# Kernel optimization log

Measured on AMD Instinct MI355X. Metric: run time of the kernel, lower is better.

The kernel has to match this reference:

```python
import jax, jax.numpy as jnp
import numpy as np

H = 8           # hidden_size
IN = 1          # input_size
OUT = 1         # output_size
T_IN = 512      # input_length
T_OUT = 128     # output_length
B = 65536       # batch


def _gru_cell(x, h, W_ih, W_hh, b_ih, b_hh):
    # torch.nn.GRUCell math. x: [B, D], h: [B, H]
    gi = x @ W_ih.T + b_ih          # [B, 3H]
    gh = h @ W_hh.T + b_hh          # [B, 3H]
    i_r, i_z, i_n = jnp.split(gi, 3, axis=-1)
    h_r, h_z, h_n = jnp.split(gh, 3, axis=-1)
    r = jax.nn.sigmoid(i_r + h_r)
    z = jax.nn.sigmoid(i_z + h_z)
    n = jnp.tanh(i_n + r * h_n)
    return (1.0 - z) * n + z * h


def setup_inputs() -> dict:
    key = jax.random.key(0)
    ks = jax.random.split(key, 12)
    s_in = 1.0 / np.sqrt(H)
    x = jax.random.normal(ks[0], (T_IN, B, IN), dtype=jnp.float32)
    u = lambda k, shp: jax.random.uniform(k, shp, dtype=jnp.float32, minval=-s_in, maxval=s_in)
    return {
        "x": x,
        "enc_W_ih": u(ks[1], (3 * H, IN)),
        "enc_W_hh": u(ks[2], (3 * H, H)),
        "enc_b_ih": u(ks[3], (3 * H,)),
        "enc_b_hh": u(ks[4], (3 * H,)),
        "dec_W_ih": u(ks[5], (3 * H, OUT)),
        "dec_W_hh": u(ks[6], (3 * H, H)),
        "dec_b_ih": u(ks[7], (3 * H,)),
        "dec_b_hh": u(ks[8], (3 * H,)),
        "fc_W": u(ks[9], (OUT, H)),
        "fc_b": u(ks[10], (OUT,)),
    }


def reference(x, enc_W_ih, enc_W_hh, enc_b_ih, enc_b_hh,
              dec_W_ih, dec_W_hh, dec_b_ih, dec_b_hh, fc_W, fc_b):
    batch = x.shape[1]
    h0 = jnp.zeros((batch, H), dtype=x.dtype)

    def enc_step(h, x_t):
        return _gru_cell(x_t, h, enc_W_ih, enc_W_hh, enc_b_ih, enc_b_hh), None

    enc_h, _ = jax.lax.scan(enc_step, h0, x)

    def dec_step(carry, _):
        h, inp = carry
        h = _gru_cell(inp, h, dec_W_ih, dec_W_hh, dec_b_ih, dec_b_hh)
        out_t = h @ fc_W.T + fc_b      # [B, OUT]
        return (h, out_t), out_t

    # decoder_feat is None, teacher_forcing False: feed back own prediction
    _, outs = jax.lax.scan(dec_step, (enc_h, x[-1]), None, length=T_OUT)
    return outs  # [T_OUT, B, OUT]
```

## Files before the change

### kernel.cpp

```cpp
#include <hip/hip_runtime.h>

#define T_IN   512
#define T_OUT  128
#define BATCH  65536

typedef float v2f __attribute__((ext_vector_type(2)));

__device__ __forceinline__ float exp2_fast(float v) { return __builtin_amdgcn_exp2f(v); }
__device__ __forceinline__ float rcp_fast(float v)  { return __builtin_amdgcn_rcpf(v); }

__device__ __forceinline__ v2f pk_fma(v2f a, v2f b, v2f c) {
    v2f d;
    asm("v_pk_fma_f32 %0, %1, %2, %3" : "=v"(d) : "v"(a), "v"(b), "v"(c));
    return d;
}

template<int CTRL>
__device__ __forceinline__ float dppf(float v) {
    return __int_as_float(__builtin_amdgcn_mov_dpp(__float_as_int(v), CTRL, 0xF, 0xF, false));
}
#define QP_XOR1 0xB1
#define QP_XOR2 0x4E
#define QP_XOR3 0x1B
#define HALF_MIRROR 0x141

__global__ __launch_bounds__(256, 4) void gru_seq2seq(
    const float* __restrict__ x,
    const float* __restrict__ eWih, const float* __restrict__ eWhh,
    const float* __restrict__ eBih, const float* __restrict__ eBhh,
    const float* __restrict__ dWih, const float* __restrict__ dWhh,
    const float* __restrict__ dBih, const float* __restrict__ dBhh,
    const float* __restrict__ fcW,  const float* __restrict__ fcB,
    float* __restrict__ out)
{
    const int tid = threadIdx.x;
    const int u   = tid & 7;
    const int e0  = (int)blockIdx.x * 64 + (tid >> 3);

    const float CR = -1.44269504088896340736f;
    const float CN =  2.88539008177792681472f;

    v2f wr[8], wz[8], wn[8];
    v2f wirv, wizv, winv;
    v2f brv, bzv, bnv, binv;

    auto dup = [](float v) { return v2f{v, v}; };

    auto load_w = [&](const float* Wih, const float* Whh,
                      const float* Bih, const float* Bhh) {
        #pragma unroll
        for (int d = 0; d < 8; ++d) {
            const int c = u ^ d;
            wr[d] = dup(Whh[u*8      + c] * CR);
            wz[d] = dup(Whh[(u+8)*8  + c] * CR);
            wn[d] = dup(Whh[(u+16)*8 + c] * CN);
        }
        wirv = dup(Wih[u]    * CR);
        wizv = dup(Wih[u+8]  * CR);
        winv = dup(Wih[u+16] * CN);
        brv  = dup((Bih[u]   + Bhh[u])   * CR);
        bzv  = dup((Bih[u+8] + Bhh[u+8]) * CR);
        bnv  = dup(Bhh[u+16] * CN);
        binv = dup(Bih[u+16] * CN);
    };

    load_w(eWih, eWhh, eBih, eBhh);

    const v2f C_NEG2 = {-2.f, -2.f};
    const v2f C_ONE  = { 1.f,  1.f};

    v2f hp[8];
    #pragma unroll
    for (int d = 0; d < 8; ++d) hp[d] = v2f{0.f, 0.f};

    auto cell2 = [&](v2f xp) {
        v2f ar = brv, az = bzv, an = bnv;
        #pragma unroll
        for (int d = 0; d < 8; ++d) {
            ar = pk_fma(wr[d], hp[d], ar);
            az = pk_fma(wz[d], hp[d], az);
            an = pk_fma(wn[d], hp[d], an);
        }
        const v2f sr = pk_fma(xp, wirv, ar);
        const v2f sz = pk_fma(xp, wizv, az);

        const float er0 = exp2_fast(sr.x), er1 = exp2_fast(sr.y);
        const float ez0 = exp2_fast(sz.x), ez1 = exp2_fast(sz.y);
        const float dr0 = 1.0f + er0, dr1 = 1.0f + er1;
        const float dz0 = 1.0f + ez0, dz1 = 1.0f + ez1;
        const float P0  = dr0 * dz0,  P1  = dr1 * dz1;
        const float rp  = rcp_fast(P0 * P1);
        const float rpA = rp * P1,    rpB = rp * P0;
        const v2f r01 = { dz0 * rpA, dz1 * rpB };
        const v2f z01 = { dr0 * rpA, dr1 * rpB };

        v2f pre = pk_fma(xp, winv, binv);
        pre = pk_fma(r01, an, pre);
        const float en0 = exp2_fast(pre.x), en1 = exp2_fast(pre.y);
        const float Dn0 = 1.0f + en0, Dn1 = 1.0f + en1;
        const float rpn = rcp_fast(Dn0 * Dn1);
        const v2f rn  = { rpn * Dn1, rpn * Dn0 };
        const v2f n01 = pk_fma(C_NEG2, rn, C_ONE);

        const v2f hm = hp[0] - n01;
        hp[0] = pk_fma(z01, hm, n01);

        const float g0 = hp[0].x, g1 = hp[0].y;
        float a7x = dppf<HALF_MIRROR>(g0);
        float a7y = dppf<HALF_MIRROR>(g1);
        hp[1] = v2f{ dppf<QP_XOR1>(g0), dppf<QP_XOR1>(g1) };
        hp[2] = v2f{ dppf<QP_XOR2>(g0), dppf<QP_XOR2>(g1) };
        hp[3] = v2f{ dppf<QP_XOR3>(g0), dppf<QP_XOR3>(g1) };
        hp[7] = v2f{ a7x, a7y };
        hp[6] = v2f{ dppf<QP_XOR1>(a7x), dppf<QP_XOR1>(a7y) };
        hp[5] = v2f{ dppf<QP_XOR2>(a7x), dppf<QP_XOR2>(a7y) };
        hp[4] = v2f{ dppf<QP_XOR3>(a7x), dppf<QP_XOR3>(a7y) };
    };

    const float* xp = x + e0;
    v2f xa0 = { xp[0],     xp[32] };
    v2f xa1 = { xp[BATCH], xp[BATCH + 32] };
    xp += 2 * (size_t)BATCH;
    #pragma unroll 2
    for (int t = 0; t < T_IN - 2; ++t) {
        const v2f xa2 = { xp[0], xp[32] };
        xp += BATCH;
        cell2(xa0);
        xa0 = xa1; xa1 = xa2;
    }
    cell2(xa0);
    cell2(xa1);

    load_w(dWih, dWhh, dBih, dBhh);
    v2f fw[8];
    #pragma unroll
    for (int d = 0; d < 8; ++d) fw[d] = dup(fcW[u ^ d]);
    const v2f fbv = dup(fcB[0]);

    v2f inp = xa1;
    float* outp = out + e0;
    #pragma unroll 1
    for (int t = 0; t < T_OUT; ++t) {
        cell2(inp);
        v2f ay = fbv;
        #pragma unroll
        for (int d = 0; d < 8; ++d) ay = pk_fma(fw[d], hp[d], ay);
        if (u == 0) {
            outp[t * BATCH]      = ay.x;
            outp[t * BATCH + 32] = ay.y;
        }
        inp = ay;
    }
}

extern "C" void kernel_launch(void* const* d_in, const int* in_sizes, int n_in,
                              void* d_out, int out_size, void* d_ws, size_t ws_size,
                              hipStream_t stream) {
    const float* x    = (const float*)d_in[0];
    const float* eWih = (const float*)d_in[1];
    const float* eWhh = (const float*)d_in[2];
    const float* eBih = (const float*)d_in[3];
    const float* eBhh = (const float*)d_in[4];
    const float* dWih = (const float*)d_in[5];
    const float* dWhh = (const float*)d_in[6];
    const float* dBih = (const float*)d_in[7];
    const float* dBhh = (const float*)d_in[8];
    const float* fcW  = (const float*)d_in[9];
    const float* fcB  = (const float*)d_in[10];
    float* out = (float*)d_out;

    dim3 grid(BATCH / 64);
    dim3 block(256);
    gru_seq2seq<<<grid, block, 0, stream>>>(x, eWih, eWhh, eBih, eBhh,
                                            dWih, dWhh, dBih, dBhh,
                                            fcW, fcB, out);
}
```

Before: 382.5 us.

## Remap GRU lanes to two hidden units per lane over four-lane groups

Each batch element is now handled by a group of 4 lanes, with every lane owning 2 hidden units packed into a v2f. Before, 8 lanes each owned 1 unit for 2 batch elements. The recurrent matvec uses op_sel variants of v_pk_fma to broadcast one half of each neighbour's hidden pair. This cuts the per-step hidden-state exchange from 14 DPP moves to 6. The decoder's output projection becomes one packed multiply plus a two-step DPP reduction instead of 16 packed FMAs. The cost is a more intricate weight layout, and transcendental work per lane is unchanged.

```diff
diff --git a/kernel.cpp b/kernel.cpp
--- a/kernel.cpp
+++ b/kernel.cpp
@@ -6,12 +6,39 @@
 
 typedef float v2f __attribute__((ext_vector_type(2)));
 
+__device__ __forceinline__ float rcp_fast(float v) { return __builtin_amdgcn_rcpf(v); }
 __device__ __forceinline__ float exp2_fast(float v) { return __builtin_amdgcn_exp2f(v); }
-__device__ __forceinline__ float rcp_fast(float v)  { return __builtin_amdgcn_rcpf(v); }
 
 __device__ __forceinline__ v2f pk_fma(v2f a, v2f b, v2f c) {
     v2f d;
     asm("v_pk_fma_f32 %0, %1, %2, %3" : "=v"(d) : "v"(a), "v"(b), "v"(c));
+    return d;
+}
+__device__ __forceinline__ void pk_fma_ip(v2f& acc, v2f a, v2f b) {
+    asm("v_pk_fma_f32 %0, %1, %2, %0" : "+v"(acc) : "v"(a), "v"(b));
+}
+__device__ __forceinline__ v2f pk_mul(v2f a, v2f b) {
+    v2f d;
+    asm("v_pk_mul_f32 %0, %1, %2" : "=v"(d) : "v"(a), "v"(b));
+    return d;
+}
+__device__ __forceinline__ v2f pk_add(v2f a, v2f b) {
+    v2f d;
+    asm("v_pk_add_f32 %0, %1, %2" : "=v"(d) : "v"(a), "v"(b));
+    return d;
+}
+__device__ __forceinline__ void pk_fma_L(v2f& acc, v2f w, v2f h) {
+    asm("v_pk_fma_f32 %0, %1, %2, %0 op_sel:[0,0,0] op_sel_hi:[1,0,1]"
+        : "+v"(acc) : "v"(w), "v"(h));
+}
+__device__ __forceinline__ void pk_fma_H(v2f& acc, v2f w, v2f h) {
+    asm("v_pk_fma_f32 %0, %1, %2, %0 op_sel:[0,1,0] op_sel_hi:[1,1,1]"
+        : "+v"(acc) : "v"(w), "v"(h));
+}
+__device__ __forceinline__ v2f pk_fma_L0(v2f w, v2f h, v2f c) {
+    v2f d;
+    asm("v_pk_fma_f32 %0, %1, %2, %3 op_sel:[0,0,0] op_sel_hi:[1,0,1]"
+        : "=v"(d) : "v"(w), "v"(h), "v"(c));
     return d;
 }
 
@@ -22,7 +49,6 @@
 #define QP_XOR1 0xB1
 #define QP_XOR2 0x4E
 #define QP_XOR3 0x1B
-#define HALF_MIRROR 0x141
 
 __global__ __launch_bounds__(256, 4) void gru_seq2seq(
     const float* __restrict__ x,
@@ -34,55 +60,67 @@
     float* __restrict__ out)
 {
     const int tid = threadIdx.x;
-    const int u   = tid & 7;
-    const int e0  = (int)blockIdx.x * 64 + (tid >> 3);
+    const int u   = tid & 3;
+    const int e0  = (int)blockIdx.x * 64 + (tid >> 2);
 
     const float CR = -1.44269504088896340736f;
     const float CN =  2.88539008177792681472f;
 
+    const int r0 = 2*u, r1 = 2*u + 1;
+
     v2f wr[8], wz[8], wn[8];
-    v2f wirv, wizv, winv;
-    v2f brv, bzv, bnv, binv;
-
-    auto dup = [](float v) { return v2f{v, v}; };
+    v2f wirp, wizp, winp;
+    v2f brp, bzp, bnp, binp;
 
     auto load_w = [&](const float* Wih, const float* Whh,
                       const float* Bih, const float* Bhh) {
         #pragma unroll
-        for (int d = 0; d < 8; ++d) {
-            const int c = u ^ d;
-            wr[d] = dup(Whh[u*8      + c] * CR);
-            wz[d] = dup(Whh[(u+8)*8  + c] * CR);
-            wn[d] = dup(Whh[(u+16)*8 + c] * CN);
+        for (int m = 0; m < 4; ++m) {
+            #pragma unroll
+            for (int lh = 0; lh < 2; ++lh) {
+                const int j = 2*(u^m) + lh;
+                wr[2*m+lh] = v2f{ Whh[r0*8      + j] * CR, Whh[r1*8      + j] * CR };
+                wz[2*m+lh] = v2f{ Whh[(r0+8)*8  + j] * CR, Whh[(r1+8)*8  + j] * CR };
+                wn[2*m+lh] = v2f{ Whh[(r0+16)*8 + j] * CN, Whh[(r1+16)*8 + j] * CN };
+            }
         }
-        wirv = dup(Wih[u]    * CR);
-        wizv = dup(Wih[u+8]  * CR);
-        winv = dup(Wih[u+16] * CN);
-        brv  = dup((Bih[u]   + Bhh[u])   * CR);
-        bzv  = dup((Bih[u+8] + Bhh[u+8]) * CR);
-        bnv  = dup(Bhh[u+16] * CN);
-        binv = dup(Bih[u+16] * CN);
+        wirp = v2f{ Wih[r0]    * CR, Wih[r1]    * CR };
+        wizp = v2f{ Wih[r0+8]  * CR, Wih[r1+8]  * CR };
+        winp = v2f{ Wih[r0+16] * CN, Wih[r1+16] * CN };
+        brp  = v2f{ (Bih[r0]   + Bhh[r0])   * CR, (Bih[r1]   + Bhh[r1])   * CR };
+        bzp  = v2f{ (Bih[r0+8] + Bhh[r0+8]) * CR, (Bih[r1+8] + Bhh[r1+8]) * CR };
+        bnp  = v2f{ Bhh[r0+16] * CN,              Bhh[r1+16] * CN };
+        binp = v2f{ Bih[r0+16] * CN,              Bih[r1+16] * CN };
     };
 
     load_w(eWih, eWhh, eBih, eBhh);
 
     const v2f C_NEG2 = {-2.f, -2.f};
     const v2f C_ONE  = { 1.f,  1.f};
-
-    v2f hp[8];
+    const v2f C_HALF = { 0.5f, 0.5f};
+
+    v2f hp[4];
     #pragma unroll
-    for (int d = 0; d < 8; ++d) hp[d] = v2f{0.f, 0.f};
-
-    auto cell2 = [&](v2f xp) {
-        v2f ar = brv, az = bzv, an = bnv;
+    for (int m = 0; m < 4; ++m) hp[m] = v2f{0.f, 0.f};
+
+    auto cell = [&](v2f xv) {
+        v2f ar = pk_fma_L0(wr[0], hp[0], brp);
+        v2f az = pk_fma_L0(wz[0], hp[0], bzp);
+        v2f an = pk_fma_L0(wn[0], hp[0], bnp);
+        pk_fma_H(ar, wr[1], hp[0]);
+        pk_fma_H(az, wz[1], hp[0]);
+        pk_fma_H(an, wn[1], hp[0]);
         #pragma unroll
-        for (int d = 0; d < 8; ++d) {
-            ar = pk_fma(wr[d], hp[d], ar);
-            az = pk_fma(wz[d], hp[d], az);
-            an = pk_fma(wn[d], hp[d], an);
+        for (int m = 1; m < 4; ++m) {
+            pk_fma_L(ar, wr[2*m],   hp[m]);
+            pk_fma_L(az, wz[2*m],   hp[m]);
+            pk_fma_L(an, wn[2*m],   hp[m]);
+            pk_fma_H(ar, wr[2*m+1], hp[m]);
+            pk_fma_H(az, wz[2*m+1], hp[m]);
+            pk_fma_H(an, wn[2*m+1], hp[m]);
         }
-        const v2f sr = pk_fma(xp, wirv, ar);
-        const v2f sz = pk_fma(xp, wizv, az);
+        const v2f sr = pk_fma(xv, wirp, ar);
+        const v2f sz = pk_fma(xv, wizp, az);
 
         const float er0 = exp2_fast(sr.x), er1 = exp2_fast(sr.y);
         const float ez0 = exp2_fast(sz.x), ez1 = exp2_fast(sz.y);
@@ -94,7 +132,7 @@
         const v2f r01 = { dz0 * rpA, dz1 * rpB };
         const v2f z01 = { dr0 * rpA, dr1 * rpB };
 
-        v2f pre = pk_fma(xp, winv, binv);
+        v2f pre = pk_fma(xv, winp, binp);
         pre = pk_fma(r01, an, pre);
         const float en0 = exp2_fast(pre.x), en1 = exp2_fast(pre.y);
         const float Dn0 = 1.0f + en0, Dn1 = 1.0f + en1;
@@ -102,54 +140,44 @@
         const v2f rn  = { rpn * Dn1, rpn * Dn0 };
         const v2f n01 = pk_fma(C_NEG2, rn, C_ONE);
 
-        const v2f hm = hp[0] - n01;
+        const v2f hm = pk_fma(n01, C_NEG2 * C_HALF , hp[0]);
         hp[0] = pk_fma(z01, hm, n01);
 
         const float g0 = hp[0].x, g1 = hp[0].y;
-        float a7x = dppf<HALF_MIRROR>(g0);
-        float a7y = dppf<HALF_MIRROR>(g1);
         hp[1] = v2f{ dppf<QP_XOR1>(g0), dppf<QP_XOR1>(g1) };
         hp[2] = v2f{ dppf<QP_XOR2>(g0), dppf<QP_XOR2>(g1) };
         hp[3] = v2f{ dppf<QP_XOR3>(g0), dppf<QP_XOR3>(g1) };
-        hp[7] = v2f{ a7x, a7y };
-        hp[6] = v2f{ dppf<QP_XOR1>(a7x), dppf<QP_XOR1>(a7y) };
-        hp[5] = v2f{ dppf<QP_XOR2>(a7x), dppf<QP_XOR2>(a7y) };
-        hp[4] = v2f{ dppf<QP_XOR3>(a7x), dppf<QP_XOR3>(a7y) };
     };
 
     const float* xp = x + e0;
-    v2f xa0 = { xp[0],     xp[32] };
-    v2f xa1 = { xp[BATCH], xp[BATCH + 32] };
+    float x0 = xp[0];
+    float x1 = xp[BATCH];
     xp += 2 * (size_t)BATCH;
     #pragma unroll 2
     for (int t = 0; t < T_IN - 2; ++t) {
-        const v2f xa2 = { xp[0], xp[32] };
-        xp += BATCH;
-        cell2(xa0);
-        xa0 = xa1; xa1 = xa2;
+        const float x2 = *xp; xp += BATCH;
+        cell(v2f{x0, x0});
+        x0 = x1; x1 = x2;
     }
-    cell2(xa0);
-    cell2(xa1);
+    cell(v2f{x0, x0});
+    cell(v2f{x1, x1});
 
     load_w(dWih, dWhh, dBih, dBhh);
-    v2f fw[8];
-    #pragma unroll
-    for (int d = 0; d < 8; ++d) fw[d] = dup(fcW[u ^ d]);
-    const v2f fbv = dup(fcB[0]);
-
-    v2f inp = xa1;
+    const v2f fwp = v2f{ fcW[r0], fcW[r1] };
+    const float fb = fcB[0];
+
+    float inp = x1;
     float* outp = out + e0;
     #pragma unroll 1
     for (int t = 0; t < T_OUT; ++t) {
-        cell2(inp);
-        v2f ay = fbv;
-        #pragma unroll
-        for (int d = 0; d < 8; ++d) ay = pk_fma(fw[d], hp[d], ay);
-        if (u == 0) {
-            outp[t * BATCH]      = ay.x;
-            outp[t * BATCH + 32] = ay.y;
-        }
-        inp = ay;
+        cell(v2f{inp, inp});
+        const v2f ay = pk_mul(fwp, hp[0]);
+        float s = ay.x + ay.y;
+        s += dppf<QP_XOR1>(s);
+        s += dppf<QP_XOR2>(s);
+        const float y = s + fb;
+        if (u == 0) outp[t * BATCH] = y;
+        inp = y;
     }
 }
 
```

New measurement: 345.2 us. -9.8%, faster.
